# Performance work log

Measured on AMD Instinct MI355X. Metric: run time of the kernel, lower is better.

## Reference

```python
import jax, jax.numpy as jnp
import numpy as np

BN_EPS = 1e-5

def setup_inputs() -> dict:
    key = jax.random.key(0)
    k1, k2, k3, k4 = jax.random.split(key, 4)
    B, V, DI, DO = 4096, 64, 128, 128
    feat = jax.random.normal(k1, (B, V, DI), dtype=jnp.float32)
    adj = jax.random.uniform(k2, (V, V), dtype=jnp.float32)
    # per-vertex Linear weights (stacked): W[v] maps dim_in -> dim_out
    W = jax.random.normal(k3, (V, DI, DO), dtype=jnp.float32) * (1.0 / np.sqrt(DI))
    b = jax.random.normal(k4, (V, DO), dtype=jnp.float32) * 0.01
    gamma = jnp.ones((V, DO), dtype=jnp.float32)
    beta = jnp.zeros((V, DO), dtype=jnp.float32)
    return {"feat": feat, "adj": adj, "W": W, "b": b, "gamma": gamma, "beta": beta}

def reference(feat, adj, W, b, gamma, beta):
    # Per-vertex Linear as one grouped GEMM: [B,V,DI] x [V,DI,DO] -> [B,V,DO]
    h = jnp.einsum('bvi,vio->bvo', feat, W) + b[None, :, :]
    # BatchNorm1d (training mode): normalize over batch dim, per vertex & channel
    mu = jnp.mean(h, axis=0, keepdims=True)            # [1,V,DO]
    var = jnp.mean((h - mu) ** 2, axis=0, keepdims=True)  # biased variance
    h = (h - mu) * jax.lax.rsqrt(var + BN_EPS) * gamma[None] + beta[None]
    # adjacency mix: adj [V,V] applied to every batch element, then relu
    out = jnp.einsum('uv,bvo->buo', adj, h)
    return jax.nn.relu(out)
```

## Files before the change

### kernel.cpp

```cpp
#include <hip/hip_runtime.h>

#define BN 4096
#define VN 64
#define DI 128
#define DO 128

typedef __attribute__((ext_vector_type(8))) short short8;
typedef __attribute__((ext_vector_type(4))) float f32x4;

__device__ __forceinline__ float bf2f(unsigned short s) {
    return __uint_as_float(((unsigned)s) << 16);
}
__device__ __forceinline__ unsigned short f2bf(float f) {
    unsigned u = __float_as_uint(f);
    u += 0x7FFF + ((u >> 16) & 1);
    return (unsigned short)(u >> 16);
}
__device__ __forceinline__ unsigned pack_bf16_trunc(float lo, float hi) {
    return __builtin_amdgcn_perm(__float_as_uint(hi), __float_as_uint(lo), 0x07060302u);
}

__global__ __launch_bounds__(256) void k_prep(const float* __restrict__ W,
                                              const float* __restrict__ adj,
                                              unsigned short* __restrict__ Wt,
                                              unsigned short* __restrict__ adjbf) {
    const int t = threadIdx.x, blk = blockIdx.x;
    if (blk < 512) {
        const int v = blk >> 3, q = blk & 7;
        const float* Wv = W + (size_t)v * DI * DO;
        unsigned short* Wtv = Wt + (size_t)v * DI * DO;
        const int o = t & 127;
        const int i0 = q * 16 + (t >> 7) * 8;
        short8 s0;
#pragma unroll
        for (int j = 0; j < 8; ++j)
            s0[j] = (short)f2bf(Wv[(size_t)(i0 + j) * DO + o]);
        *(short8*)(Wtv + o * DI + i0) = s0;
    } else {
        short8 s0, s1;
#pragma unroll
        for (int j = 0; j < 8; ++j) s0[j] = (short)f2bf(adj[t * 16 + j]);
#pragma unroll
        for (int j = 0; j < 8; ++j) s1[j] = (short)f2bf(adj[t * 16 + 8 + j]);
        *(short8*)(adjbf + t * 16) = s0;
        *(short8*)(adjbf + t * 16 + 8) = s1;
    }
}

__global__ __launch_bounds__(256) void k_gemm1(const float* __restrict__ feat,
                                               const unsigned short* __restrict__ Wt,
                                               const float* __restrict__ bias,
                                               unsigned short* __restrict__ h,
                                               float* __restrict__ psA,
                                               float* __restrict__ psB) {
    const int bt = blockIdx.x;
    const int v = blockIdx.y;
    const int tid = threadIdx.x;
    const int w = tid >> 6, lane = tid & 63;
    const int wm = w >> 1, wn = w & 1;
    const int quad = lane >> 4, l16 = lane & 15;

    size_t aidx[4];
#pragma unroll
    for (int rt = 0; rt < 4; ++rt)
        aidx[rt] = (size_t)(bt * 128 + wm * 64 + rt * 16 + l16) * (VN * DI)
                 + v * DI + quad * 8;

    short8 bb[4][4];
#pragma unroll
    for (int ks = 0; ks < 4; ++ks)
#pragma unroll
        for (int nt = 0; nt < 4; ++nt)
            bb[ks][nt] = *(const short8*)(Wt + (size_t)v * (DI * DO)
                                          + (size_t)(wn * 64 + nt * 16 + l16) * DI
                                          + quad * 8 + ks * 32);

    f32x4 acc[4][4];
#pragma unroll
    for (int rt = 0; rt < 4; ++rt)
#pragma unroll
        for (int nt = 0; nt < 4; ++nt) acc[rt][nt] = (f32x4){0.f, 0.f, 0.f, 0.f};

#define LOADA(dst, k0)                                                        \
    {                                                                         \
        _Pragma("unroll") for (int rt = 0; rt < 4; ++rt) {                    \
            f32x4 f0 = *(const f32x4*)(feat + aidx[rt] + (k0));               \
            f32x4 f1 = *(const f32x4*)(feat + aidx[rt] + (k0) + 4);          \
            union { short8 s; unsigned u[4]; } pk;                            \
            pk.u[0] = pack_bf16_trunc(f0[0], f0[1]);                          \
            pk.u[1] = pack_bf16_trunc(f0[2], f0[3]);                          \
            pk.u[2] = pack_bf16_trunc(f1[0], f1[1]);                          \
            pk.u[3] = pack_bf16_trunc(f1[2], f1[3]);                          \
            dst[rt] = pk.s;                                                   \
        }                                                                     \
    }

    short8 aCur[4], aNxt[4];
    LOADA(aCur, 0)
#pragma unroll
    for (int ks = 0; ks < 4; ++ks) {
        if (ks < 3) LOADA(aNxt, (ks + 1) * 32)
#pragma unroll
        for (int rt = 0; rt < 4; ++rt)
#pragma unroll
            for (int nt = 0; nt < 4; ++nt)
                acc[rt][nt] = __builtin_amdgcn_mfma_f32_16x16x32_bf16(
                    aCur[rt], bb[ks][nt], acc[rt][nt], 0, 0, 0);
#pragma unroll
        for (int rt = 0; rt < 4; ++rt) aCur[rt] = aNxt[rt];
    }
#undef LOADA

#pragma unroll
    for (int nt = 0; nt < 4; ++nt) {
        const int col = wn * 64 + nt * 16 + l16;
        const float bv = bias[v * DO + col];
        float s = 0.f, sq = 0.f;
#pragma unroll
        for (int rt = 0; rt < 4; ++rt)
#pragma unroll
            for (int e = 0; e < 4; ++e) {
                float x = acc[rt][nt][e] + bv;
                acc[rt][nt][e] = x;
                s += x;
                sq += x * x;
            }
        s += __shfl_down(s, 32);  s += __shfl_down(s, 16);
        sq += __shfl_down(sq, 32); sq += __shfl_down(sq, 16);
        if (lane < 16) {
            const size_t pi = ((size_t)(v * 32 + bt) * 2 + wm) * 128 + col;
            psA[pi] = s;
            psB[pi] = sq;
        }
#pragma unroll
        for (int rt = 0; rt < 4; ++rt)
#pragma unroll
            for (int e = 0; e < 4; ++e) {
                int brow = bt * 128 + wm * 64 + rt * 16 + quad * 4 + e;
                h[(size_t)brow * (VN * DO) + v * DO + col] = f2bf(acc[rt][nt][e]);
            }
    }
}

__global__ __launch_bounds__(128) void k_reduce(const float* __restrict__ psA,
                                                const float* __restrict__ psB,
                                                const float* __restrict__ gamma,
                                                const float* __restrict__ beta,
                                                float* __restrict__ scale,
                                                float* __restrict__ shift) {
    const int o = threadIdx.x;
    const int v = blockIdx.x;
    float s = 0.f, sq = 0.f;
#pragma unroll
    for (int p = 0; p < 64; ++p) {
        const size_t pi = ((size_t)v * 64 + p) * 128 + o;
        s += psA[pi];
        sq += psB[pi];
    }
    const float invB = 1.0f / (float)BN;
    const float mu = s * invB;
    const float var = sq * invB - mu * mu;
    const float sc = gamma[v * DO + o] * rsqrtf(var + 1e-5f);
    scale[v * DO + o] = sc;
    shift[v * DO + o] = beta[v * DO + o] - mu * sc;
}

__global__ __launch_bounds__(128) void k_c0(const float* __restrict__ adj,
                                            const float* __restrict__ shift,
                                            float* __restrict__ C0) {
    const int o = threadIdx.x;
    const int u = blockIdx.x;
    float c0 = 0.f;
#pragma unroll
    for (int v = 0; v < VN; ++v)
        c0 += adj[u * VN + v] * shift[v * DO + o];
    C0[u * DO + o] = c0;
}

__global__ __launch_bounds__(256) void k_mix(const unsigned short* __restrict__ h,
                                             const float* __restrict__ scale,
                                             const unsigned short* __restrict__ adjbf,
                                             const float* __restrict__ C0,
                                             float* __restrict__ out) {
    __shared__ unsigned short hsT[2][DO][72];
    const int t = threadIdx.x;
    const int b0 = blockIdx.x * 2;

    const int sv = t & 63;
#pragma unroll
    for (int c = 0; c < 8; ++c) {
        const int bl = c >> 2;
        const int o0 = ((t >> 6) << 3) + (c & 3) * 32;
        short8 hv = *(const short8*)(h + ((size_t)(b0 + bl) * VN + sv) * DO + o0);
        f32x4 s0 = *(const f32x4*)(scale + sv * DO + o0);
        f32x4 s1 = *(const f32x4*)(scale + sv * DO + o0 + 4);
#pragma unroll
        for (int j = 0; j < 4; ++j)
            hsT[bl][o0 + j][sv] = f2bf(bf2f((unsigned short)hv[j]) * s0[j]);
#pragma unroll
        for (int j = 0; j < 4; ++j)
            hsT[bl][o0 + 4 + j][sv] = f2bf(bf2f((unsigned short)hv[4 + j]) * s1[j]);
    }
    __syncthreads();

    const int w = t >> 6, lane = t & 63;
    const int bl = w >> 1, nh = w & 1;
    const int quad = lane >> 4, l16 = lane & 15;
    const int b = b0 + bl;

    short8 af[4][2];
#pragma unroll
    for (int mt = 0; mt < 4; ++mt)
#pragma unroll
        for (int ks = 0; ks < 2; ++ks)
            af[mt][ks] = *(const short8*)(adjbf + (mt * 16 + l16) * VN
                                          + ks * 32 + quad * 8);

    f32x4 acc[4][4];
#pragma unroll
    for (int mt = 0; mt < 4; ++mt)
#pragma unroll
        for (int nt = 0; nt < 4; ++nt) acc[mt][nt] = (f32x4){0.f, 0.f, 0.f, 0.f};

#pragma unroll
    for (int nt = 0; nt < 4; ++nt) {
        const unsigned short* bp = &hsT[bl][nh * 64 + nt * 16 + l16][quad * 8];
        short8 bf0 = *(const short8*)(bp);
        short8 bf1 = *(const short8*)(bp + 32);
#pragma unroll
        for (int mt = 0; mt < 4; ++mt) {
            acc[mt][nt] = __builtin_amdgcn_mfma_f32_16x16x32_bf16(
                af[mt][0], bf0, acc[mt][nt], 0, 0, 0);
            acc[mt][nt] = __builtin_amdgcn_mfma_f32_16x16x32_bf16(
                af[mt][1], bf1, acc[mt][nt], 0, 0, 0);
        }
    }

#pragma unroll
    for (int mt = 0; mt < 4; ++mt)
#pragma unroll
        for (int nt = 0; nt < 4; ++nt) {
            const int o = nh * 64 + nt * 16 + l16;
#pragma unroll
            for (int e = 0; e < 4; ++e) {
                const int u = mt * 16 + quad * 4 + e;
                out[((size_t)b * VN + u) * DO + o] =
                    fmaxf(acc[mt][nt][e] + C0[u * DO + o], 0.0f);
            }
        }
}

extern "C" void kernel_launch(void* const* d_in, const int* in_sizes, int n_in,
                              void* d_out, int out_size, void* d_ws, size_t ws_size,
                              hipStream_t stream) {
    const float* feat  = (const float*)d_in[0];
    const float* adj   = (const float*)d_in[1];
    const float* W     = (const float*)d_in[2];
    const float* bias  = (const float*)d_in[3];
    const float* gamma = (const float*)d_in[4];
    const float* beta  = (const float*)d_in[5];
    float* out = (float*)d_out;

    char* ws = (char*)d_ws;
    unsigned short* h     = (unsigned short*)ws;
    unsigned short* Wt    = (unsigned short*)(ws + 67108864ull);
    unsigned short* adjbf = (unsigned short*)(ws + 69206016ull);
    float* psA   = (float*)(ws + 69214208ull);
    float* psB   = psA + 524288;
    float* scale = psB + 524288;
    float* shift = scale + 8192;
    float* C0    = shift + 8192;

    k_prep<<<dim3(513), dim3(256), 0, stream>>>(W, adj, Wt, adjbf);
    k_gemm1<<<dim3(32, 64), dim3(256), 0, stream>>>(feat, Wt, bias, h, psA, psB);
    k_reduce<<<dim3(64), dim3(128), 0, stream>>>(psA, psB, gamma, beta, scale, shift);
    k_c0<<<dim3(64), dim3(128), 0, stream>>>(adj, shift, C0);
    k_mix<<<dim3(2048), dim3(256), 0, stream>>>(h, scale, adjbf, C0, out);
}
```

Before: 340.7 us.

## Store GEMM1 output in MFMA fragment layout and widen mix blocks to four batches

GEMM1 now writes h in a blocked layout matching its MFMA accumulator fragments, using packed 8-byte stores instead of scattered 2-byte stores. The grid order is swapped so consecutive blocks cover different vertices of the same batch tile. k_mix is reworked to handle four batch elements per 512-thread block and reads the fragment-ordered h directly when building its transposed LDS tile. This is meant to cut uncoalesced write traffic in GEMM1. In exchange, the mix kernel's gather has a more complex address pattern, its LDS footprint doubles, and it scatters 2-byte LDS writes that may hit bank conflicts.

After: 298.9 us. 12.3% less time.

```diff
diff --git a/kernel.cpp b/kernel.cpp
--- a/kernel.cpp
+++ b/kernel.cpp
@@ -19,6 +19,10 @@
 __device__ __forceinline__ unsigned pack_bf16_trunc(float lo, float hi) {
     return __builtin_amdgcn_perm(__float_as_uint(hi), __float_as_uint(lo), 0x07060302u);
 }
+__device__ __forceinline__ unsigned pack_bf16_rne(float lo, float hi) {
+    return (unsigned)f2bf(lo) | ((unsigned)f2bf(hi) << 16);
+}
+
 
 __global__ __launch_bounds__(256) void k_prep(const float* __restrict__ W,
                                               const float* __restrict__ adj,
@@ -53,8 +57,8 @@
                                                unsigned short* __restrict__ h,
                                                float* __restrict__ psA,
                                                float* __restrict__ psB) {
-    const int bt = blockIdx.x;
-    const int v = blockIdx.y;
+    const int v = blockIdx.x;
+    const int bt = blockIdx.y;
     const int tid = threadIdx.x;
     const int w = tid >> 6, lane = tid & 63;
     const int wm = w >> 1, wn = w & 1;
@@ -111,6 +115,7 @@
     }
 #undef LOADA
 
+    unsigned short* hblk = h + ((size_t)(bt * 64 + v) * 4 + w) * 4096;
 #pragma unroll
     for (int nt = 0; nt < 4; ++nt) {
         const int col = wn * 64 + nt * 16 + l16;
@@ -133,12 +138,12 @@
             psB[pi] = sq;
         }
 #pragma unroll
-        for (int rt = 0; rt < 4; ++rt)
-#pragma unroll
-            for (int e = 0; e < 4; ++e) {
-                int brow = bt * 128 + wm * 64 + rt * 16 + quad * 4 + e;
-                h[(size_t)brow * (VN * DO) + v * DO + col] = f2bf(acc[rt][nt][e]);
-            }
+        for (int rt = 0; rt < 4; ++rt) {
+            uint2 pk;
+            pk.x = pack_bf16_rne(acc[rt][nt][0], acc[rt][nt][1]);
+            pk.y = pack_bf16_rne(acc[rt][nt][2], acc[rt][nt][3]);
+            *(uint2*)(hblk + (size_t)((nt * 4 + rt) * 64 + lane) * 4) = pk;
+        }
     }
 }
 
@@ -177,29 +182,31 @@
     C0[u * DO + o] = c0;
 }
 
-__global__ __launch_bounds__(256) void k_mix(const unsigned short* __restrict__ h,
-                                             const float* __restrict__ scale,
-                                             const unsigned short* __restrict__ adjbf,
-                                             const float* __restrict__ C0,
-                                             float* __restrict__ out) {
-    __shared__ unsigned short hsT[2][DO][72];
+__global__ __launch_bounds__(512, 4) void k_mix(const unsigned short* __restrict__ h,
+                                                const float* __restrict__ scale,
+                                                const unsigned short* __restrict__ adjbf,
+                                                const float* __restrict__ C0,
+                                                float* __restrict__ out) {
+    __shared__ unsigned short hsT[4][DO][72];
     const int t = threadIdx.x;
-    const int b0 = blockIdx.x * 2;
-
-    const int sv = t & 63;
-#pragma unroll
-    for (int c = 0; c < 8; ++c) {
-        const int bl = c >> 2;
-        const int o0 = ((t >> 6) << 3) + (c & 3) * 32;
-        short8 hv = *(const short8*)(h + ((size_t)(b0 + bl) * VN + sv) * DO + o0);
-        f32x4 s0 = *(const f32x4*)(scale + sv * DO + o0);
-        f32x4 s1 = *(const f32x4*)(scale + sv * DO + o0 + 4);
-#pragma unroll
-        for (int j = 0; j < 4; ++j)
-            hsT[bl][o0 + j][sv] = f2bf(bf2f((unsigned short)hv[j]) * s0[j]);
-#pragma unroll
-        for (int j = 0; j < 4; ++j)
-            hsT[bl][o0 + 4 + j][sv] = f2bf(bf2f((unsigned short)hv[4 + j]) * s1[j]);
+    const int b0 = blockIdx.x * 4;
+    const int bt = b0 >> 7;
+    const int r = b0 & 127;
+    const int swm = r >> 6, srt = (r >> 4) & 3, squad = (r >> 2) & 3;
+
+#pragma unroll
+    for (int c = 0; c < 16; ++c) {
+        const int p = c * 512 + t;
+        const int v = p >> 7, o = p & 127;
+        const size_t off = (size_t)(bt * 64 + v) * 16384
+                         + (size_t)(((swm * 2 + (o >> 6)) * 4 + ((o >> 4) & 3)) * 4 + srt) * 256
+                         + (size_t)(squad * 16 + (o & 15)) * 4;
+        const uint2 pk = *(const uint2*)(h + off);
+        const float sc = scale[v * DO + o];
+        hsT[0][o][v] = f2bf(bf2f((unsigned short)(pk.x & 0xFFFF)) * sc);
+        hsT[1][o][v] = f2bf(bf2f((unsigned short)(pk.x >> 16)) * sc);
+        hsT[2][o][v] = f2bf(bf2f((unsigned short)(pk.y & 0xFFFF)) * sc);
+        hsT[3][o][v] = f2bf(bf2f((unsigned short)(pk.y >> 16)) * sc);
     }
     __syncthreads();
 
@@ -272,8 +279,8 @@
     float* C0    = shift + 8192;
 
     k_prep<<<dim3(513), dim3(256), 0, stream>>>(W, adj, Wt, adjbf);
-    k_gemm1<<<dim3(32, 64), dim3(256), 0, stream>>>(feat, Wt, bias, h, psA, psB);
+    k_gemm1<<<dim3(64, 32), dim3(256), 0, stream>>>(feat, Wt, bias, h, psA, psB);
     k_reduce<<<dim3(64), dim3(128), 0, stream>>>(psA, psB, gamma, beta, scale, shift);
     k_c0<<<dim3(64), dim3(128), 0, stream>>>(adj, shift, C0);
-    k_mix<<<dim3(2048), dim3(256), 0, stream>>>(h, scale, adjbf, C0, out);
-}
+    k_mix<<<dim3(1024), dim3(512), 0, stream>>>(h, scale, adjbf, C0, out);
+}
```
